# Performance work log

Measured on AMD Instinct MI355X. Metric: run time of the kernel, lower is better.

The kernel has to match this reference:

```python
import jax, jax.numpy as jnp
import numpy as np

D_MODEL = 2048
NUM_EXPERTS = 64
TOP_K = 2


def setup_inputs() -> dict:
    key = jax.random.key(0)
    k_x, k_w = jax.random.split(key)
    x = jax.random.normal(k_x, (4, 8192, D_MODEL), dtype=jnp.float32)
    # nn.Linear(d_model, num_experts, bias=False): weight [num_experts, d_model]
    bound = 1.0 / np.sqrt(D_MODEL)
    W = jax.random.uniform(k_w, (NUM_EXPERTS, D_MODEL), dtype=jnp.float32,
                           minval=-bound, maxval=bound)
    return {"x": x, "W": W}


def reference(x, W):
    # router_logits = x @ W.T : [b, s, num_experts]
    logits = jnp.einsum("bsd,ed->bse", x, W)
    probs = jax.nn.softmax(logits, axis=-1)
    gates, indices = jax.lax.top_k(probs, TOP_K)  # [b, s, top_k]
    gates = gates / jnp.sum(gates, axis=-1, keepdims=True)
    return gates, indices
```

## Files before the change

kernel.cpp:

```cpp
#include <hip/hip_runtime.h>
#include <math.h>
#include <stdint.h>

#define D_MODEL 2048
#define NEXP    64
#define TOKENS  32768
#define BM      64
#define BK      64
#define NT      256
#define NCHUNK  (D_MODEL / BK)

typedef __attribute__((address_space(3))) uint32_t       lds_u32_t;
typedef const __attribute__((address_space(1))) uint32_t gbl_u32_t;

#define STAGE(c, b)                                                           \
    _Pragma("unroll")                                                         \
    for (int g = 0; g < 4; ++g) {                                             \
        const int G_ = 4 * wave + g;                                          \
        __builtin_amdgcn_global_load_lds((gbl_u32_t*)(xsrc[g] + (c) * BK),    \
                                         (lds_u32_t*)&xs[b][4 * G_][0], 16, 0, 0); \
        __builtin_amdgcn_global_load_lds((gbl_u32_t*)(wsrc[g] + (c) * BK),    \
                                         (lds_u32_t*)&ws[b][4 * G_][0], 16, 0, 0); \
    }

__global__ __launch_bounds__(NT, 2)
void router_kernel(const float* __restrict__ x, const float* __restrict__ W,
                   float* __restrict__ out)
{
    __shared__ float xs[2][BM][BK];
    __shared__ float ws[2][NEXP][BK];

    const int tid  = threadIdx.x;
    const int lane = tid & 63;
    const int wave = tid >> 6;
    const int row0 = blockIdx.x * BM;

    const int ec = tid & 15;
    const int tr = tid >> 4;

    const int lrow  = lane >> 4;
    const int lslot = lane & 15;
    const float* xsrc[4];
    const float* wsrc[4];
#pragma unroll
    for (int g = 0; g < 4; ++g) {
        const int r   = 16 * wave + 4 * g + lrow;
        const int col = 4 * (lslot ^ (r & 7));
        xsrc[g] = x + (size_t)(row0 + r) * D_MODEL + col;
        wsrc[g] = W + (size_t)r * D_MODEL + col;
    }

    float acc[4][4];
#pragma unroll
    for (int i = 0; i < 4; ++i)
#pragma unroll
        for (int j = 0; j < 4; ++j) acc[i][j] = 0.f;

    STAGE(0, 0);
    __syncthreads();

    const int trs = tr & 7;
    const int ecs = ec & 7;

    for (int c = 0; c < NCHUNK; ++c) {
        const int buf = c & 1;
        if (c + 1 < NCHUNK) { STAGE(c + 1, buf ^ 1); }
#pragma unroll
        for (int q = 0; q < BK / 4; ++q) {
            const int sA = 4 * (q ^ trs);
            const int sB = 4 * (q ^ ecs);
            float4 a[4], b[4];
#pragma unroll
            for (int i = 0; i < 4; ++i)
                a[i] = *(const float4*)&xs[buf][tr + 16 * i][sA];
#pragma unroll
            for (int j = 0; j < 4; ++j)
                b[j] = *(const float4*)&ws[buf][ec + 16 * j][sB];
#pragma unroll
            for (int i = 0; i < 4; ++i)
#pragma unroll
                for (int j = 0; j < 4; ++j) {
                    acc[i][j] = fmaf(a[i].x, b[j].x, acc[i][j]);
                    acc[i][j] = fmaf(a[i].y, b[j].y, acc[i][j]);
                    acc[i][j] = fmaf(a[i].z, b[j].z, acc[i][j]);
                    acc[i][j] = fmaf(a[i].w, b[j].w, acc[i][j]);
                }
        }
        __syncthreads();
    }

    float* logits = &xs[0][0][0];
#pragma unroll
    for (int i = 0; i < 4; ++i)
#pragma unroll
        for (int j = 0; j < 4; ++j)
            logits[(ec + 16 * j) * BM + (tr + 16 * i)] = acc[i][j];
    __syncthreads();

    if (tid < BM) {
        const int t = tid;
        float m1 = -INFINITY, m2 = -INFINITY;
        int i1 = 0, i2 = 0;
#pragma unroll 8
        for (int e = 0; e < NEXP; ++e) {
            float v = logits[e * BM + t];
            if (v > m1)      { m2 = m1; i2 = i1; m1 = v; i1 = e; }
            else if (v > m2) { m2 = v; i2 = e; }
        }
        float ex = expf(m2 - m1);
        float g1 = 1.0f / (1.0f + ex);
        float g2 = ex * g1;
        const int row = row0 + t;
        out[(size_t)row * 2 + 0] = g1;
        out[(size_t)row * 2 + 1] = g2;
        out[(size_t)TOKENS * 2 + (size_t)row * 2 + 0] = (float)i1;
        out[(size_t)TOKENS * 2 + (size_t)row * 2 + 1] = (float)i2;
    }
}

extern "C" void kernel_launch(void* const* d_in, const int* in_sizes, int n_in,
                              void* d_out, int out_size, void* d_ws, size_t ws_size,
                              hipStream_t stream) {
    const float* x = (const float*)d_in[0];
    const float* W = (const float*)d_in[1];
    float* out = (float*)d_out;
    router_kernel<<<TOKENS / BM, NT, 0, stream>>>(x, W, out);
}
```

Baseline: 152.8 us.

## Use split-bf16 MFMA for router GEMM with fp32 recompute on near-ties

Replaces the scalar fp32 FMA GEMM with bf16 MFMA 16x16x32 instructions. Each fp32 operand is split into high and low bf16 parts and four products are accumulated to approximate fp32 precision. Loads now go through registers with conversion before the LDS write, which drops the direct global-to-LDS path and adds an extra barrier per chunk. Tokens whose top-3 logits lie within a threshold are recomputed exactly in fp32 so the expert selection stays correct, at the cost of serialized per-token block work when such near-ties occur.

```diff
diff --git a/kernel.cpp b/kernel.cpp
--- a/kernel.cpp
+++ b/kernel.cpp
@@ -9,108 +9,187 @@
 #define BK      64
 #define NT      256
 #define NCHUNK  (D_MODEL / BK)
-
-typedef __attribute__((address_space(3))) uint32_t       lds_u32_t;
-typedef const __attribute__((address_space(1))) uint32_t gbl_u32_t;
-
-#define STAGE(c, b)                                                           \
-    _Pragma("unroll")                                                         \
-    for (int g = 0; g < 4; ++g) {                                             \
-        const int G_ = 4 * wave + g;                                          \
-        __builtin_amdgcn_global_load_lds((gbl_u32_t*)(xsrc[g] + (c) * BK),    \
-                                         (lds_u32_t*)&xs[b][4 * G_][0], 16, 0, 0); \
-        __builtin_amdgcn_global_load_lds((gbl_u32_t*)(wsrc[g] + (c) * BK),    \
-                                         (lds_u32_t*)&ws[b][4 * G_][0], 16, 0, 0); \
-    }
+#define TIE_THR 1e-3f
+
+typedef __attribute__((ext_vector_type(8))) short short8;
+typedef __attribute__((ext_vector_type(4))) short short4v;
+typedef __attribute__((ext_vector_type(4))) float f32x4;
+
+__device__ __forceinline__ unsigned short bf16r(float v) {
+    uint32_t u = __float_as_uint(v);
+    return (unsigned short)((u + 0x7fffu + ((u >> 16) & 1u)) >> 16);
+}
+__device__ __forceinline__ float bf2f(unsigned short h) {
+    return __uint_as_float(((uint32_t)h) << 16);
+}
+
+
+#define LOAD_CHUNK(c)                                                     \
+    _Pragma("unroll")                                                     \
+    for (int j = 0; j < 4; ++j) {                                         \
+        rx[j] = *(const float4*)(xp[j] + (size_t)(c) * BK);               \
+        rw[j] = *(const float4*)(wp[j] + (size_t)(c) * BK);               \
+    }
+
+#define CVT_WRITE(b)                                                      \
+    do {                                                                  \
+        char* base_ = smem + 32768 * (b);                                 \
+        _Pragma("unroll")                                                 \
+        for (int j = 0; j < 4; ++j) {                                     \
+            short4v h_, l_;                                               \
+            unsigned short t_;                                            \
+            t_ = bf16r(rx[j].x); h_.x = (short)t_; l_.x = (short)bf16r(rx[j].x - bf2f(t_)); \
+            t_ = bf16r(rx[j].y); h_.y = (short)t_; l_.y = (short)bf16r(rx[j].y - bf2f(t_)); \
+            t_ = bf16r(rx[j].z); h_.z = (short)t_; l_.z = (short)bf16r(rx[j].z - bf2f(t_)); \
+            t_ = bf16r(rx[j].w); h_.w = (short)t_; l_.w = (short)bf16r(rx[j].w - bf2f(t_)); \
+            *(short4v*)(base_ +     0 + wr_off[j]) = h_;                  \
+            *(short4v*)(base_ +  8192 + wr_off[j]) = l_;                  \
+            t_ = bf16r(rw[j].x); h_.x = (short)t_; l_.x = (short)bf16r(rw[j].x - bf2f(t_)); \
+            t_ = bf16r(rw[j].y); h_.y = (short)t_; l_.y = (short)bf16r(rw[j].y - bf2f(t_)); \
+            t_ = bf16r(rw[j].z); h_.z = (short)t_; l_.z = (short)bf16r(rw[j].z - bf2f(t_)); \
+            t_ = bf16r(rw[j].w); h_.w = (short)t_; l_.w = (short)bf16r(rw[j].w - bf2f(t_)); \
+            *(short4v*)(base_ + 16384 + wr_off[j]) = h_;                  \
+            *(short4v*)(base_ + 24576 + wr_off[j]) = l_;                  \
+        }                                                                 \
+    } while (0)
+
+#define MFMA_BUF(b)                                                       \
+    do {                                                                  \
+        const char* base_ = smem + 32768 * (b);                           \
+        _Pragma("unroll")                                                 \
+        for (int st = 0; st < 2; ++st) {                                  \
+            short8 ah_ = *(const short8*)(base_ +    0 + a_off[st]);      \
+            short8 al_ = *(const short8*)(base_ + 8192 + a_off[st]);      \
+            _Pragma("unroll")                                             \
+            for (int n = 0; n < 4; ++n) {                                 \
+                short8 bh_ = *(const short8*)(base_ + 16384 + b_off[n][st]); \
+                short8 bl_ = *(const short8*)(base_ + 24576 + b_off[n][st]); \
+                acc[n] = __builtin_amdgcn_mfma_f32_16x16x32_bf16(ah_, bh_, acc[n], 0, 0, 0); \
+                acc[n] = __builtin_amdgcn_mfma_f32_16x16x32_bf16(al_, bh_, acc[n], 0, 0, 0); \
+                acc[n] = __builtin_amdgcn_mfma_f32_16x16x32_bf16(ah_, bl_, acc[n], 0, 0, 0); \
+                acc[n] = __builtin_amdgcn_mfma_f32_16x16x32_bf16(al_, bl_, acc[n], 0, 0, 0); \
+            }                                                             \
+        }                                                                 \
+    } while (0)
 
 __global__ __launch_bounds__(NT, 2)
 void router_kernel(const float* __restrict__ x, const float* __restrict__ W,
                    float* __restrict__ out)
 {
-    __shared__ float xs[2][BM][BK];
-    __shared__ float ws[2][NEXP][BK];
+    __shared__ char smem[65536];
+    __shared__ int  flaglist[BM];
+    __shared__ int  nflag;
 
     const int tid  = threadIdx.x;
     const int lane = tid & 63;
     const int wave = tid >> 6;
     const int row0 = blockIdx.x * BM;
 
-    const int ec = tid & 15;
-    const int tr = tid >> 4;
-
-    const int lrow  = lane >> 4;
-    const int lslot = lane & 15;
-    const float* xsrc[4];
-    const float* wsrc[4];
-#pragma unroll
-    for (int g = 0; g < 4; ++g) {
-        const int r   = 16 * wave + 4 * g + lrow;
-        const int col = 4 * (lslot ^ (r & 7));
-        xsrc[g] = x + (size_t)(row0 + r) * D_MODEL + col;
-        wsrc[g] = W + (size_t)r * D_MODEL + col;
-    }
-
-    float acc[4][4];
-#pragma unroll
-    for (int i = 0; i < 4; ++i)
-#pragma unroll
-        for (int j = 0; j < 4; ++j) acc[i][j] = 0.f;
-
-    STAGE(0, 0);
+    const int tr0 = tid >> 4;
+    const int sl  = tid & 15;
+    const float* xp[4];
+    const float* wp[4];
+    int wr_off[4];
+#pragma unroll
+    for (int j = 0; j < 4; ++j) {
+        const int r = tr0 + 16 * j;
+        xp[j] = x + (size_t)(row0 + r) * D_MODEL + 4 * sl;
+        wp[j] = W + (size_t)r * D_MODEL + 4 * sl;
+        wr_off[j] = r * 128 + 16 * ((sl >> 1) ^ (r & 7)) + 8 * (sl & 1);
+    }
+
+    const int fr = lane & 15;
+    const int fg = lane >> 4;
+    int a_off[2], b_off[4][2];
+#pragma unroll
+    for (int st = 0; st < 2; ++st) {
+        const int ar = 16 * wave + fr;
+        a_off[st] = ar * 128 + 16 * (((st << 2) + fg) ^ (ar & 7));
+#pragma unroll
+        for (int n = 0; n < 4; ++n) {
+            const int br = 16 * n + fr;
+            b_off[n][st] = br * 128 + 16 * (((st << 2) + fg) ^ (br & 7));
+        }
+    }
+
+    f32x4 acc[4];
+#pragma unroll
+    for (int n = 0; n < 4; ++n) acc[n] = (f32x4){0.f, 0.f, 0.f, 0.f};
+
+    float4 rx[4], rw[4];
+    LOAD_CHUNK(0);
+    CVT_WRITE(0);
     __syncthreads();
-
-    const int trs = tr & 7;
-    const int ecs = ec & 7;
 
     for (int c = 0; c < NCHUNK; ++c) {
         const int buf = c & 1;
-        if (c + 1 < NCHUNK) { STAGE(c + 1, buf ^ 1); }
-#pragma unroll
-        for (int q = 0; q < BK / 4; ++q) {
-            const int sA = 4 * (q ^ trs);
-            const int sB = 4 * (q ^ ecs);
-            float4 a[4], b[4];
-#pragma unroll
-            for (int i = 0; i < 4; ++i)
-                a[i] = *(const float4*)&xs[buf][tr + 16 * i][sA];
-#pragma unroll
-            for (int j = 0; j < 4; ++j)
-                b[j] = *(const float4*)&ws[buf][ec + 16 * j][sB];
-#pragma unroll
-            for (int i = 0; i < 4; ++i)
-#pragma unroll
-                for (int j = 0; j < 4; ++j) {
-                    acc[i][j] = fmaf(a[i].x, b[j].x, acc[i][j]);
-                    acc[i][j] = fmaf(a[i].y, b[j].y, acc[i][j]);
-                    acc[i][j] = fmaf(a[i].z, b[j].z, acc[i][j]);
-                    acc[i][j] = fmaf(a[i].w, b[j].w, acc[i][j]);
-                }
-        }
-        __syncthreads();
-    }
-
-    float* logits = &xs[0][0][0];
-#pragma unroll
-    for (int i = 0; i < 4; ++i)
-#pragma unroll
-        for (int j = 0; j < 4; ++j)
-            logits[(ec + 16 * j) * BM + (tr + 16 * i)] = acc[i][j];
+        if (c + 1 < NCHUNK) { LOAD_CHUNK(c + 1); }
+        MFMA_BUF(buf);
+        __syncthreads();
+        if (c + 1 < NCHUNK) { CVT_WRITE(buf ^ 1); }
+        __syncthreads();
+    }
+
+    float* logits = (float*)smem;
+#pragma unroll
+    for (int n = 0; n < 4; ++n)
+#pragma unroll
+        for (int r = 0; r < 4; ++r)
+            logits[(16 * wave + 4 * fg + r) * 66 + 16 * n + fr] = acc[n][r];
+    if (tid == 0) nflag = 0;
     __syncthreads();
 
+    float m1 = -INFINITY, m2 = -INFINITY, m3 = -INFINITY;
+    int   i1 = 0, i2 = 0;
+    bool  tie = false;
     if (tid < BM) {
-        const int t = tid;
-        float m1 = -INFINITY, m2 = -INFINITY;
-        int i1 = 0, i2 = 0;
 #pragma unroll 8
         for (int e = 0; e < NEXP; ++e) {
-            float v = logits[e * BM + t];
-            if (v > m1)      { m2 = m1; i2 = i1; m1 = v; i1 = e; }
-            else if (v > m2) { m2 = v; i2 = e; }
-        }
-        float ex = expf(m2 - m1);
-        float g1 = 1.0f / (1.0f + ex);
-        float g2 = ex * g1;
-        const int row = row0 + t;
+            const float v = logits[tid * 66 + e];
+            if (v > m1)      { m3 = m2; m2 = m1; i2 = i1; m1 = v; i1 = e; }
+            else if (v > m2) { m3 = m2; m2 = v; i2 = e; }
+            else if (v > m3) { m3 = v; }
+        }
+        tie = (m1 - m2 < TIE_THR) || (m2 - m3 < TIE_THR);
+        if (tie) { const int p = atomicAdd(&nflag, 1); flaglist[p] = tid; }
+    }
+    __syncthreads();
+
+    const int nf = nflag;
+    float* partial = (float*)(smem + 32768);
+    for (int f = 0; f < nf; ++f) {
+        const int t = flaglist[f];
+        const float* xr = x + (size_t)(row0 + t) * D_MODEL + 512 * wave;
+        const float* wrow = W + (size_t)lane * D_MODEL + 512 * wave;
+        float ps = 0.f;
+        for (int k = 0; k < 512; k += 4) {
+            const float4 xv = *(const float4*)(xr + k);
+            const float4 wv = *(const float4*)(wrow + k);
+            ps = fmaf(xv.x, wv.x, ps); ps = fmaf(xv.y, wv.y, ps);
+            ps = fmaf(xv.z, wv.z, ps); ps = fmaf(xv.w, wv.w, ps);
+        }
+        partial[wave * 64 + lane] = ps;
+        __syncthreads();
+        if (tid < NEXP)
+            logits[t * 66 + tid] = (partial[tid] + partial[64 + tid]) +
+                                   (partial[128 + tid] + partial[192 + tid]);
+        __syncthreads();
+    }
+
+    if (tid < BM) {
+        if (tie) {
+            m1 = -INFINITY; m2 = -INFINITY; i1 = 0; i2 = 0;
+#pragma unroll 8
+            for (int e = 0; e < NEXP; ++e) {
+                const float v = logits[tid * 66 + e];
+                if (v > m1)      { m2 = m1; i2 = i1; m1 = v; i1 = e; }
+                else if (v > m2) { m2 = v; i2 = e; }
+            }
+        }
+        const float ex = expf(m2 - m1);
+        const float g1 = 1.0f / (1.0f + ex);
+        const float g2 = ex * g1;
+        const int row = row0 + tid;
         out[(size_t)row * 2 + 0] = g1;
         out[(size_t)row * 2 + 1] = g2;
         out[(size_t)TOKENS * 2 + (size_t)row * 2 + 0] = (float)i1;
```

After: 190.0 us. 24.4% more time.

## Use split-bf16 MFMA for router GEMM with exact FP32 recompute on near ties

Applied to the files above, without the earlier changes.

Replaces the scalar FP32 FMA inner loop with bf16 MFMA 16x16x32 instructions, splitting each float into high and low bf16 parts and issuing three MFMAs to approximate FP32 precision. Tokens whose top-3 logits lie within a small threshold of each other are flagged and their logits recomputed exactly in FP32 from global memory, which keeps the top-k selection faithful. This trades the FP32 vector ALU bottleneck for matrix-core throughput, at the cost of extra split arithmetic on each LDS read and a serial per-token recompute path when ties occur.

```diff
diff --git a/kernel.cpp b/kernel.cpp
--- a/kernel.cpp
+++ b/kernel.cpp
@@ -9,19 +9,50 @@
 #define BK      64
 #define NT      256
 #define NCHUNK  (D_MODEL / BK)
+#define TIE_THR 1e-3f
+#define LSTRIDE 66
+
+typedef __attribute__((ext_vector_type(8))) short short8;
+typedef __attribute__((ext_vector_type(4))) float f32x4;
+typedef __attribute__((ext_vector_type(4))) int   i32x4;
 
 typedef __attribute__((address_space(3))) uint32_t       lds_u32_t;
 typedef const __attribute__((address_space(1))) uint32_t gbl_u32_t;
 
-#define STAGE(c, b)                                                           \
-    _Pragma("unroll")                                                         \
-    for (int g = 0; g < 4; ++g) {                                             \
-        const int G_ = 4 * wave + g;                                          \
-        __builtin_amdgcn_global_load_lds((gbl_u32_t*)(xsrc[g] + (c) * BK),    \
+#define STAGE(c, b)                                                            \
+    _Pragma("unroll")                                                          \
+    for (int g = 0; g < 4; ++g) {                                              \
+        const int G_ = 4 * wave + g;                                           \
+        __builtin_amdgcn_global_load_lds((gbl_u32_t*)(xsrc[g] + (size_t)(c) * BK), \
                                          (lds_u32_t*)&xs[b][4 * G_][0], 16, 0, 0); \
-        __builtin_amdgcn_global_load_lds((gbl_u32_t*)(wsrc[g] + (c) * BK),    \
+        __builtin_amdgcn_global_load_lds((gbl_u32_t*)(wsrc[g] + (size_t)(c) * BK), \
                                          (lds_u32_t*)&ws[b][4 * G_][0], 16, 0, 0); \
     }
+
+__device__ __forceinline__ void split2(float f0, float f1, uint32_t& hw, uint32_t& lw)
+{
+    const uint32_t u0 = __float_as_uint(f0), u1 = __float_as_uint(f1);
+    const uint32_t a0 = u0 & 0xffff0000u,  a1 = u1 & 0xffff0000u;
+    hw = a1 | (u0 >> 16);
+    const float l0 = f0 - __uint_as_float(a0);
+    const float l1 = f1 - __uint_as_float(a1);
+    lw = (__float_as_uint(l1) & 0xffff0000u) | (__float_as_uint(l0) >> 16);
+}
+
+__device__ __forceinline__ void ldsplit(const char* p0, const char* p1,
+                                        short8& h8, short8& l8)
+{
+    const float4 qa = *(const float4*)p0;
+    const float4 qb = *(const float4*)p1;
+    i32x4 hv, lv;
+    uint32_t hw, lw;
+    split2(qa.x, qa.y, hw, lw); hv[0] = (int)hw; lv[0] = (int)lw;
+    split2(qa.z, qa.w, hw, lw); hv[1] = (int)hw; lv[1] = (int)lw;
+    split2(qb.x, qb.y, hw, lw); hv[2] = (int)hw; lv[2] = (int)lw;
+    split2(qb.z, qb.w, hw, lw); hv[3] = (int)hw; lv[3] = (int)lw;
+    h8 = *(short8*)&hv;
+    l8 = *(short8*)&lv;
+}
 
 __global__ __launch_bounds__(NT, 2)
 void router_kernel(const float* __restrict__ x, const float* __restrict__ W,
@@ -29,14 +60,13 @@
 {
     __shared__ float xs[2][BM][BK];
     __shared__ float ws[2][NEXP][BK];
+    __shared__ int   flaglist[BM];
+    __shared__ int   nflag;
 
     const int tid  = threadIdx.x;
     const int lane = tid & 63;
     const int wave = tid >> 6;
     const int row0 = blockIdx.x * BM;
-
-    const int ec = tid & 15;
-    const int tr = tid >> 4;
 
     const int lrow  = lane >> 4;
     const int lslot = lane & 15;
@@ -50,67 +80,110 @@
         wsrc[g] = W + (size_t)r * D_MODEL + col;
     }
 
-    float acc[4][4];
-#pragma unroll
-    for (int i = 0; i < 4; ++i)
-#pragma unroll
-        for (int j = 0; j < 4; ++j) acc[i][j] = 0.f;
+    const int fr  = lane & 15;
+    const int h   = lane >> 4;
+    const int sw  = 16 * (fr & 7);
+    const int t0b = (32 * h) ^ sw;
+    const int mt0 = 2 * (wave & 1);
+    const int nt0 = 2 * (wave >> 1);
+    const int rowA[2] = { (16 * (mt0 + 0) + fr) * 256, (16 * (mt0 + 1) + fr) * 256 };
+    const int rowB[2] = { (16 * (nt0 + 0) + fr) * 256, (16 * (nt0 + 1) + fr) * 256 };
+
+    f32x4 acc[2][2] = {};
 
     STAGE(0, 0);
     __syncthreads();
 
-    const int trs = tr & 7;
-    const int ecs = ec & 7;
-
     for (int c = 0; c < NCHUNK; ++c) {
         const int buf = c & 1;
-        if (c + 1 < NCHUNK) { STAGE(c + 1, buf ^ 1); }
-#pragma unroll
-        for (int q = 0; q < BK / 4; ++q) {
-            const int sA = 4 * (q ^ trs);
-            const int sB = 4 * (q ^ ecs);
-            float4 a[4], b[4];
-#pragma unroll
-            for (int i = 0; i < 4; ++i)
-                a[i] = *(const float4*)&xs[buf][tr + 16 * i][sA];
-#pragma unroll
-            for (int j = 0; j < 4; ++j)
-                b[j] = *(const float4*)&ws[buf][ec + 16 * j][sB];
-#pragma unroll
-            for (int i = 0; i < 4; ++i)
-#pragma unroll
-                for (int j = 0; j < 4; ++j) {
-                    acc[i][j] = fmaf(a[i].x, b[j].x, acc[i][j]);
-                    acc[i][j] = fmaf(a[i].y, b[j].y, acc[i][j]);
-                    acc[i][j] = fmaf(a[i].z, b[j].z, acc[i][j]);
-                    acc[i][j] = fmaf(a[i].w, b[j].w, acc[i][j]);
+        if (c + 1 < NCHUNK) STAGE(c + 1, buf ^ 1);
+        const char* xb = (const char*)&xs[buf][0][0];
+        const char* wb = (const char*)&ws[buf][0][0];
+#pragma unroll
+        for (int s = 0; s < 2; ++s) {
+            const int off0 = 128 * s + t0b;
+            short8 ah[2], al[2], bh[2], bl[2];
+#pragma unroll
+            for (int mi = 0; mi < 2; ++mi)
+                ldsplit(xb + rowA[mi] + off0, xb + rowA[mi] + (off0 ^ 16), ah[mi], al[mi]);
+#pragma unroll
+            for (int ni = 0; ni < 2; ++ni)
+                ldsplit(wb + rowB[ni] + off0, wb + rowB[ni] + (off0 ^ 16), bh[ni], bl[ni]);
+#pragma unroll
+            for (int mi = 0; mi < 2; ++mi)
+#pragma unroll
+                for (int ni = 0; ni < 2; ++ni) {
+                    acc[mi][ni] = __builtin_amdgcn_mfma_f32_16x16x32_bf16(ah[mi], bh[ni], acc[mi][ni], 0, 0, 0);
+                    acc[mi][ni] = __builtin_amdgcn_mfma_f32_16x16x32_bf16(al[mi], bh[ni], acc[mi][ni], 0, 0, 0);
+                    acc[mi][ni] = __builtin_amdgcn_mfma_f32_16x16x32_bf16(ah[mi], bl[ni], acc[mi][ni], 0, 0, 0);
                 }
         }
         __syncthreads();
     }
 
-    float* logits = &xs[0][0][0];
-#pragma unroll
-    for (int i = 0; i < 4; ++i)
-#pragma unroll
-        for (int j = 0; j < 4; ++j)
-            logits[(ec + 16 * j) * BM + (tr + 16 * i)] = acc[i][j];
+    float* logits = (float*)&xs[0][0][0];
+#pragma unroll
+    for (int mi = 0; mi < 2; ++mi)
+#pragma unroll
+        for (int ni = 0; ni < 2; ++ni)
+#pragma unroll
+            for (int r = 0; r < 4; ++r)
+                logits[(16 * (mt0 + mi) + 4 * h + r) * LSTRIDE + 16 * (nt0 + ni) + fr] =
+                    acc[mi][ni][r];
+    if (tid == 0) nflag = 0;
     __syncthreads();
 
+    float m1 = -INFINITY, m2 = -INFINITY, m3 = -INFINITY;
+    int   i1 = 0, i2 = 0;
+    bool  tie = false;
     if (tid < BM) {
-        const int t = tid;
-        float m1 = -INFINITY, m2 = -INFINITY;
-        int i1 = 0, i2 = 0;
 #pragma unroll 8
         for (int e = 0; e < NEXP; ++e) {
-            float v = logits[e * BM + t];
-            if (v > m1)      { m2 = m1; i2 = i1; m1 = v; i1 = e; }
-            else if (v > m2) { m2 = v; i2 = e; }
-        }
-        float ex = expf(m2 - m1);
-        float g1 = 1.0f / (1.0f + ex);
-        float g2 = ex * g1;
-        const int row = row0 + t;
+            const float v = logits[tid * LSTRIDE + e];
+            if (v > m1)      { m3 = m2; m2 = m1; i2 = i1; m1 = v; i1 = e; }
+            else if (v > m2) { m3 = m2; m2 = v; i2 = e; }
+            else if (v > m3) { m3 = v; }
+        }
+        tie = (m1 - m2 < TIE_THR) || (m2 - m3 < TIE_THR);
+        if (tie) { const int p = atomicAdd(&nflag, 1); flaglist[p] = tid; }
+    }
+    __syncthreads();
+
+    const int nf = nflag;
+    float* partial = (float*)&ws[0][0][0];
+    for (int f = 0; f < nf; ++f) {
+        const int t = flaglist[f];
+        const float* xr   = x + (size_t)(row0 + t) * D_MODEL + 512 * wave;
+        const float* wrow = W + (size_t)lane * D_MODEL + 512 * wave;
+        float ps = 0.f;
+        for (int k = 0; k < 512; k += 4) {
+            const float4 xv = *(const float4*)(xr + k);
+            const float4 wv = *(const float4*)(wrow + k);
+            ps = fmaf(xv.x, wv.x, ps); ps = fmaf(xv.y, wv.y, ps);
+            ps = fmaf(xv.z, wv.z, ps); ps = fmaf(xv.w, wv.w, ps);
+        }
+        partial[wave * 64 + lane] = ps;
+        __syncthreads();
+        if (tid < NEXP)
+            logits[t * LSTRIDE + tid] = (partial[tid] + partial[64 + tid]) +
+                                        (partial[128 + tid] + partial[192 + tid]);
+        __syncthreads();
+    }
+
+    if (tid < BM) {
+        if (tie) {
+            m1 = -INFINITY; m2 = -INFINITY; i1 = 0; i2 = 0;
+#pragma unroll 8
+            for (int e = 0; e < NEXP; ++e) {
+                const float v = logits[tid * LSTRIDE + e];
+                if (v > m1)      { m2 = m1; i2 = i1; m1 = v; i1 = e; }
+                else if (v > m2) { m2 = v; i2 = e; }
+            }
+        }
+        const float ex = expf(m2 - m1);
+        const float g1 = 1.0f / (1.0f + ex);
+        const float g2 = ex * g1;
+        const int row = row0 + tid;
         out[(size_t)row * 2 + 0] = g1;
         out[(size_t)row * 2 + 1] = g2;
         out[(size_t)TOKENS * 2 + (size_t)row * 2 + 0] = (float)i1;
```

New measurement: 179.0 us. 1.17x slower.
